# Performance work log

Hardware: AMD Instinct MI355X
Metric: run time of the kernel (lower is better)

The kernel has to match this reference:

```python
import jax, jax.numpy as jnp
import numpy as np

N_EMBD = 1024
N_HEAD = 16
HEAD_DIM = N_EMBD // N_HEAD
D_FF = 4 * N_EMBD
B, T = 2, 2048


def setup_inputs() -> dict:
    key = jax.random.key(0)
    ks = jax.random.split(key, 16)
    s = 0.02
    d = {
        'x': jax.random.normal(ks[0], (B, T, N_EMBD), jnp.float32),
        'ln1_g': jnp.ones((N_EMBD,), jnp.float32),
        'ln1_b': jnp.zeros((N_EMBD,), jnp.float32),
        'Wq': jax.random.normal(ks[1], (N_EMBD, N_EMBD), jnp.float32) * s,
        'bq': jnp.zeros((N_EMBD,), jnp.float32),
        'Wk': jax.random.normal(ks[2], (N_EMBD, N_EMBD), jnp.float32) * s,
        'bk': jnp.zeros((N_EMBD,), jnp.float32),
        'Wv': jax.random.normal(ks[3], (N_EMBD, N_EMBD), jnp.float32) * s,
        'bv': jnp.zeros((N_EMBD,), jnp.float32),
        'Wo': jax.random.normal(ks[4], (N_EMBD, N_EMBD), jnp.float32) * s,
        'bo': jnp.zeros((N_EMBD,), jnp.float32),
        'ln2_g': jnp.ones((N_EMBD,), jnp.float32),
        'ln2_b': jnp.zeros((N_EMBD,), jnp.float32),
        'W1': jax.random.normal(ks[5], (N_EMBD, D_FF), jnp.float32) * s,
        'b1': jnp.zeros((D_FF,), jnp.float32),
        'W2': jax.random.normal(ks[6], (D_FF, N_EMBD), jnp.float32) * s,
        'b2': jnp.zeros((N_EMBD,), jnp.float32),
    }
    return d


def _layernorm(x, g, b, eps=1e-5):
    mu = jnp.mean(x, axis=-1, keepdims=True)
    var = jnp.var(x, axis=-1, keepdims=True)
    return (x - mu) * jax.lax.rsqrt(var + eps) * g + b


def _attention(x, Wq, bq, Wk, bk, Wv, bv, Wo, bo):
    b, t, c = x.shape
    q = (x @ Wq + bq).reshape(b, t, N_HEAD, HEAD_DIM).transpose(0, 2, 1, 3)
    k = (x @ Wk + bk).reshape(b, t, N_HEAD, HEAD_DIM).transpose(0, 2, 1, 3)
    v = (x @ Wv + bv).reshape(b, t, N_HEAD, HEAD_DIM).transpose(0, 2, 1, 3)
    att = jnp.einsum('bhqd,bhkd->bhqk', q, k) / jnp.sqrt(jnp.float32(HEAD_DIM))
    causal = jnp.tril(jnp.ones((t, t), bool))
    att = jnp.where(causal[None, None], att, -jnp.inf)
    att = jax.nn.softmax(att, axis=-1)
    y = jnp.einsum('bhqk,bhkd->bhqd', att, v)
    y = y.transpose(0, 2, 1, 3).reshape(b, t, c)
    return y @ Wo + bo


def reference(x, ln1_g, ln1_b, Wq, bq, Wk, bk, Wv, bv, Wo, bo, ln2_g, ln2_b, W1, b1, W2, b2):
    x = x + _attention(_layernorm(x, ln1_g, ln1_b), Wq, bq, Wk, bk, Wv, bv, Wo, bo)
    h = _layernorm(x, ln2_g, ln2_b)
    h = jax.nn.gelu(h @ W1 + b1, approximate=False) @ W2 + b2
    return x + h
```

## Files before the change

kernel.cpp:

```cpp
#include <hip/hip_runtime.h>
#include <hip/hip_bf16.h>

typedef __hip_bfloat16 bf16;
using bf16x8 = __attribute__((ext_vector_type(8))) short;
using f32x4  = __attribute__((ext_vector_type(4))) float;
using f32x16 = __attribute__((ext_vector_type(16))) float;
using u32x4  = __attribute__((ext_vector_type(4))) unsigned int;

#define TSEQ 2048
#define NH   16
#define HD   64
#define NC   1024
#define DFF  4096
#define NROWS 4096

__device__ __forceinline__ void load_lds16(const bf16* g, bf16* l) {
  __builtin_amdgcn_global_load_lds(
      (const __attribute__((address_space(1))) unsigned int*)g,
      (__attribute__((address_space(3))) unsigned int*)l, 16, 0, 0);
}

__device__ __forceinline__ float b2f(short s) {
  unsigned int u = ((unsigned int)(unsigned short)s) << 16;
  return __builtin_bit_cast(float, u);
}

__device__ __forceinline__ unsigned cvtpk(float a, float b) {
  unsigned r;
  asm("v_cvt_pk_bf16_f32 %0, %1, %2" : "=v"(r) : "v"(a), "v"(b));
  return r;
}

__device__ __forceinline__ void pl32swap(unsigned &d, unsigned &s) {
  asm("v_permlane32_swap_b32 %0, %1" : "+v"(d), "+v"(s));
}

__device__ __forceinline__ float gelu_f(float x) {
  float u = 0.7978845608028654f * fmaf(0.044715f * x, x * x, x);
  float e = __expf(2.0f * u);
  float t = 1.0f - 2.0f / (e + 1.0f);
  return 0.5f * x * (1.0f + t);
}

__global__ __launch_bounds__(256)
void ln_cast_kernel(const float* __restrict__ x, const float* __restrict__ g,
                    const float* __restrict__ b, bf16* __restrict__ out) {
  int row = blockIdx.x, tid = threadIdx.x;
  const float4 v = ((const float4*)(x + (size_t)row * NC))[tid];
  float s  = v.x + v.y + v.z + v.w;
  float s2 = v.x*v.x + v.y*v.y + v.z*v.z + v.w*v.w;
#pragma unroll
  for (int m = 1; m < 64; m <<= 1) { s += __shfl_xor(s, m); s2 += __shfl_xor(s2, m); }
  __shared__ float rs[4], rs2[4];
  if ((tid & 63) == 0) { rs[tid >> 6] = s; rs2[tid >> 6] = s2; }
  __syncthreads();
  s  = rs[0] + rs[1] + rs[2] + rs[3];
  s2 = rs2[0] + rs2[1] + rs2[2] + rs2[3];
  float mu   = s * (1.0f / NC);
  float var  = s2 * (1.0f / NC) - mu * mu;
  float rstd = rsqrtf(var + 1e-5f);
  const float4 gv = ((const float4*)g)[tid];
  const float4 bv = ((const float4*)b)[tid];
  bf16* o = out + (size_t)row * NC + tid * 4;
  o[0] = __float2bfloat16((v.x - mu) * rstd * gv.x + bv.x);
  o[1] = __float2bfloat16((v.y - mu) * rstd * gv.y + bv.y);
  o[2] = __float2bfloat16((v.z - mu) * rstd * gv.z + bv.z);
  o[3] = __float2bfloat16((v.w - mu) * rstd * gv.w + bv.w);
}

__global__ __launch_bounds__(256)
void wo_ln_kernel(const float* __restrict__ x, const float* __restrict__ bo,
                  const bf16* __restrict__ P, const float* __restrict__ g,
                  const float* __restrict__ bln, float* __restrict__ x2,
                  bf16* __restrict__ xn2) {
  int row = blockIdx.x, tid = threadIdx.x;
  size_t base = (size_t)row * NC + tid * 4;
  const float4 xv = *(const float4*)(x + base);
  const float4 bv = ((const float4*)bo)[tid];
  short4 p0 = *(const short4*)((const short*)P + base);
  short4 p1 = *(const short4*)((const short*)P + (size_t)NROWS * NC + base);
  float v0 = xv.x + bv.x + b2f(p0.x) + b2f(p1.x);
  float v1 = xv.y + bv.y + b2f(p0.y) + b2f(p1.y);
  float v2 = xv.z + bv.z + b2f(p0.z) + b2f(p1.z);
  float v3 = xv.w + bv.w + b2f(p0.w) + b2f(p1.w);
  float4 ov = {v0, v1, v2, v3};
  *(float4*)(x2 + base) = ov;
  float s  = v0 + v1 + v2 + v3;
  float s2 = v0*v0 + v1*v1 + v2*v2 + v3*v3;
#pragma unroll
  for (int m = 1; m < 64; m <<= 1) { s += __shfl_xor(s, m); s2 += __shfl_xor(s2, m); }
  __shared__ float rs[4], rs2[4];
  if ((tid & 63) == 0) { rs[tid >> 6] = s; rs2[tid >> 6] = s2; }
  __syncthreads();
  s  = rs[0] + rs[1] + rs[2] + rs[3];
  s2 = rs2[0] + rs2[1] + rs2[2] + rs2[3];
  float mu   = s * (1.0f / NC);
  float var  = s2 * (1.0f / NC) - mu * mu;
  float rstd = rsqrtf(var + 1e-5f);
  const float4 gv = ((const float4*)g)[tid];
  const float4 lv = ((const float4*)bln)[tid];
  bf16* o = xn2 + base;
  o[0] = __float2bfloat16((v0 - mu) * rstd * gv.x + lv.x);
  o[1] = __float2bfloat16((v1 - mu) * rstd * gv.y + lv.y);
  o[2] = __float2bfloat16((v2 - mu) * rstd * gv.z + lv.z);
  o[3] = __float2bfloat16((v3 - mu) * rstd * gv.w + lv.w);
}

__global__ __launch_bounds__(256)
void w2_final_kernel(const float* __restrict__ x2, const float* __restrict__ b2,
                     const bf16* __restrict__ P, float* __restrict__ out) {
  int row = blockIdx.x, tid = threadIdx.x;
  size_t base = (size_t)row * NC + tid * 4;
  const float4 xv = *(const float4*)(x2 + base);
  const float4 bv = ((const float4*)b2)[tid];
  float a0 = xv.x + bv.x, a1 = xv.y + bv.y, a2 = xv.z + bv.z, a3 = xv.w + bv.w;
#pragma unroll
  for (int z = 0; z < 4; ++z) {
    short4 p = *(const short4*)((const short*)P + (size_t)z * NROWS * NC + base);
    a0 += b2f(p.x); a1 += b2f(p.y); a2 += b2f(p.z); a3 += b2f(p.w);
  }
  float4 ov = {a0, a1, a2, a3};
  *(float4*)(out + base) = ov;
}

__global__ __launch_bounds__(256)
void transpose_all_kernel(const float* __restrict__ Wq, const float* __restrict__ Wk,
                          const float* __restrict__ Wv, const float* __restrict__ Wo,
                          const float* __restrict__ W1, const float* __restrict__ W2,
                          bf16* __restrict__ WqkvoT, bf16* __restrict__ W1T,
                          bf16* __restrict__ W2T) {
  int bid = blockIdx.x;
  const float* W; bf16* Wt; int K, N, nx, tile;
  if (bid < 4096) {
    int z = bid >> 10; tile = bid & 1023;
    W = (z == 0) ? Wq : (z == 1) ? Wk : (z == 2) ? Wv : Wo;
    Wt = WqkvoT + (size_t)z * NC * NC; K = NC; N = NC; nx = 32;
  } else if (bid < 8192) {
    tile = bid - 4096; W = W1; Wt = W1T; K = NC; N = DFF; nx = 128;
  } else {
    tile = bid - 8192; W = W2; Wt = W2T; K = DFF; N = NC; nx = 32;
  }
  int n0 = (tile % nx) * 32, k0 = (tile / nx) * 32;
  __shared__ float t[32][33];
  int tx = threadIdx.x, ty = threadIdx.y;
#pragma unroll
  for (int i = 0; i < 4; ++i)
    t[ty + i * 8][tx] = W[(size_t)(k0 + ty + i * 8) * N + n0 + tx];
  __syncthreads();
#pragma unroll
  for (int i = 0; i < 4; ++i)
    Wt[(size_t)(n0 + ty + i * 8) * K + k0 + tx] = __float2bfloat16(t[tx][ty + i * 8]);
}

#define MODE_GELU 4
#define MODE_QKV  5
#define MODE_PART 6

template <int MODE>
__global__ __launch_bounds__(256)
void gemm_bt(const bf16* __restrict__ A, const bf16* __restrict__ Bt,
             const float* __restrict__ bias, const float* __restrict__ bias2,
             const float* __restrict__ bias3,
             void* __restrict__ outp, void* __restrict__ out2, void* __restrict__ out3,
             int M, int N, int K, int KS) {
  __shared__ bf16 As[128 * 64];
  __shared__ bf16 Bs[128 * 64];
  int tid  = threadIdx.x;
  int w    = tid >> 6;
  int lane = tid & 63;
  int l32  = lane & 31;
  int khalf = lane >> 5;
  int sx   = lane & 7;
  int waveM = (w >> 1) * 64, waveN = (w & 1) * 64;

  int gN = gridDim.x, gM = gridDim.y;
  int pid = blockIdx.y * gN + blockIdx.x;
  int npg = 8 * gN;
  int gid = pid / npg;
  int fm  = gid * 8;
  int gsz = min(gM - fm, 8);
  int bm = (fm + (pid % gsz)) * 128;
  int bn = ((pid % npg) / gsz) * 128;

  int k_beg = blockIdx.z * KS;

  const bf16* pA[4]; const bf16* pB[4];
#pragma unroll
  for (int i = 0; i < 4; ++i) {
    int p = i * 256 + tid;
    int row = p >> 3;
    int lc = (p & 7) ^ (row & 7);
    pA[i] = A  + (size_t)(bm + row) * K + k_beg + lc * 8;
    pB[i] = Bt + (size_t)(bn + row) * K + k_beg + lc * 8;
  }

  f32x16 acc[2][2];
#pragma unroll
  for (int mi = 0; mi < 2; ++mi)
#pragma unroll
    for (int ni = 0; ni < 2; ++ni)
#pragma unroll
      for (int r = 0; r < 16; ++r) acc[mi][ni][r] = 0.f;

  for (int kt = 0; kt < KS; kt += 64) {
    __syncthreads();
#pragma unroll
    for (int i = 0; i < 4; ++i) {
      load_lds16(pA[i], &As[(i * 256 + w * 64) * 8]);
      load_lds16(pB[i], &Bs[(i * 256 + w * 64) * 8]);
      pA[i] += 64; pB[i] += 64;
    }
    __syncthreads();
#pragma unroll
    for (int s = 0; s < 4; ++s) {
      int ch = ((s * 2 + khalf) ^ sx) * 8;
      bf16x8 af[2], bfr[2];
#pragma unroll
      for (int mi = 0; mi < 2; ++mi)
        af[mi] = *(const bf16x8*)&As[(waveM + mi * 32 + l32) * 64 + ch];
#pragma unroll
      for (int ni = 0; ni < 2; ++ni)
        bfr[ni] = *(const bf16x8*)&Bs[(waveN + ni * 32 + l32) * 64 + ch];
#pragma unroll
      for (int mi = 0; mi < 2; ++mi)
#pragma unroll
        for (int ni = 0; ni < 2; ++ni)
          acc[mi][ni] = __builtin_amdgcn_mfma_f32_32x32x16_bf16(af[mi], bfr[ni], acc[mi][ni], 0, 0, 0);
    }
  }

  if (MODE == MODE_PART) {
    bf16* dst = (bf16*)outp + (size_t)blockIdx.z * M * N;
#pragma unroll
    for (int mi = 0; mi < 2; ++mi)
#pragma unroll
      for (int ni = 0; ni < 2; ++ni) {
        int col = bn + waveN + ni * 32 + l32;
#pragma unroll
        for (int reg = 0; reg < 16; ++reg) {
          int row = bm + waveM + mi * 32 + (reg & 3) + 8 * (reg >> 2) + 4 * khalf;
          dst[(size_t)row * N + col] = __float2bfloat16(acc[mi][ni][reg]);
        }
      }
  } else if (MODE == MODE_GELU) {
    float bcol[2];
#pragma unroll
    for (int ni = 0; ni < 2; ++ni) bcol[ni] = bias[bn + waveN + ni * 32 + l32];
#pragma unroll
    for (int mi = 0; mi < 2; ++mi)
#pragma unroll
      for (int ni = 0; ni < 2; ++ni) {
        int col = bn + waveN + ni * 32 + l32;
#pragma unroll
        for (int reg = 0; reg < 16; ++reg) {
          int row = bm + waveM + mi * 32 + (reg & 3) + 8 * (reg >> 2) + 4 * khalf;
          ((bf16*)outp)[(size_t)row * N + col] =
              __float2bfloat16(gelu_f(acc[mi][ni][reg] + bcol[ni]));
        }
      }
  } else {
    int seg = bn >> 10;
    int c1b = (bn & (NC - 1)) + waveN;
    const float* bp = (seg == 0) ? bias : (seg == 1) ? bias2 : bias3;
    float bcol[2]; int hh[2], dd[2];
#pragma unroll
    for (int ni = 0; ni < 2; ++ni) {
      int c1 = c1b + ni * 32 + l32;
      bcol[ni] = bp[c1]; hh[ni] = c1 >> 6; dd[ni] = c1 & (HD - 1);
    }
    if (seg == 0) {
      bf16* dst = (bf16*)outp;
#pragma unroll
      for (int mi = 0; mi < 2; ++mi)
#pragma unroll
        for (int reg = 0; reg < 16; ++reg) {
          int row = bm + waveM + mi * 32 + (reg & 3) + 8 * (reg >> 2) + 4 * khalf;
          int bbi = row >> 11, t = row & (TSEQ - 1);
#pragma unroll
          for (int ni = 0; ni < 2; ++ni)
            dst[((size_t)(bbi * NH + hh[ni]) * TSEQ + t) * HD + dd[ni]] =
                __float2bfloat16(acc[mi][ni][reg] + bcol[ni]);
        }
    } else if (seg == 1) {
      bf16* dst = (bf16*)out2;
#pragma unroll
      for (int mi = 0; mi < 2; ++mi)
#pragma unroll
        for (int reg = 0; reg < 16; ++reg) {
          int row = bm + waveM + mi * 32 + (reg & 3) + 8 * (reg >> 2) + 4 * khalf;
          int bbi = row >> 11, t = row & (TSEQ - 1);
          int kt = t >> 5, lk = t & 31;
#pragma unroll
          for (int ni = 0; ni < 2; ++ni) {
            int d = dd[ni];
            size_t off = ((((size_t)(bbi * NH + hh[ni]) * 64 + kt) * 4 + (d >> 4)) * 64
                          + ((d >> 3) & 1) * 32 + lk) * 8 + (d & 7);
            dst[off] = __float2bfloat16(acc[mi][ni][reg] + bcol[ni]);
          }
        }
    } else {
      bf16* dst = (bf16*)out3;
#pragma unroll
      for (int mi = 0; mi < 2; ++mi)
#pragma unroll
        for (int reg = 0; reg < 16; ++reg) {
          int row = bm + waveM + mi * 32 + (reg & 3) + 8 * (reg >> 2) + 4 * khalf;
          int bbi = row >> 11, t = row & (TSEQ - 1);
          int kt = t >> 5, rem = t & 31;
          int ks = rem >> 4, hf = (rem >> 3) & 1, j = rem & 7;
#pragma unroll
          for (int ni = 0; ni < 2; ++ni) {
            int d = dd[ni];
            size_t off = (((((size_t)(bbi * NH + hh[ni]) * 64 + kt) * 2 + (d >> 5)) * 2 + ks) * 64
                          + hf * 32 + (d & 31)) * 8 + j;
            dst[off] = __float2bfloat16(acc[mi][ni][reg] + bcol[ni]);
          }
        }
    }
  }
}

__global__ __launch_bounds__(256)
void attn_kernel(const bf16* __restrict__ q, const bf16* __restrict__ kf,
                 const bf16* __restrict__ vf, bf16* __restrict__ out) {
  int id  = blockIdx.x;
  int xcd = id & 7;
  int t   = id >> 3;
  int bh  = xcd * 4 + (t & 3);
  int u   = t >> 2;
  int qt  = (u < 32) ? (2 * u) : (63 - 2 * (u - 32));
  int b = bh >> 4, h = bh & 15;

  int tid  = threadIdx.x;
  int w    = tid >> 6;
  int lane = tid & 63;
  int l31  = lane & 31;
  int hh   = lane >> 5;
  int h8   = hh * 8;
  int base4 = hh * 4;

  const bf16* qp  = q  + (size_t)(b * NH + h) * TSEQ * HD;
  const bf16* kfb = kf + (size_t)bh * (64 * 4 * 64 * 8);
  const bf16* vfb = vf + (size_t)bh * (64 * 2 * 2 * 64 * 8);

  int q0 = qt * 32;

  bf16x8 qf[4];
#pragma unroll
  for (int ds = 0; ds < 4; ++ds)
    qf[ds] = *(const bf16x8*)(qp + (size_t)(q0 + l31) * HD + ds * 16 + h8);

  f32x16 o0, o1;
#pragma unroll
  for (int r = 0; r < 16; ++r) { o0[r] = 0.f; o1[r] = 0.f; }
  float lacc = 0.f;

  bf16x8 a0, a1, a2, a3;

  auto step = [&](int kt, bool dg) {
    const bf16* vs = vfb + (size_t)kt * 2048 + lane * 8;
    bf16x8 v00 = *(const bf16x8*)(vs);
    bf16x8 v01 = *(const bf16x8*)(vs + 512);
    bf16x8 v10 = *(const bf16x8*)(vs + 1024);
    bf16x8 v11 = *(const bf16x8*)(vs + 1536);
    bf16x8 n0, n1, n2, n3;
    bool pf = !dg && (kt + 4 <= qt);
    if (pf) {
      const bf16* kn = kfb + (size_t)(kt + 4) * 2048 + lane * 8;
      n0 = *(const bf16x8*)(kn);
      n1 = *(const bf16x8*)(kn + 512);
      n2 = *(const bf16x8*)(kn + 1024);
      n3 = *(const bf16x8*)(kn + 1536);
    }

    f32x16 c;
#pragma unroll
    for (int r = 0; r < 16; ++r) c[r] = 0.f;
    c = __builtin_amdgcn_mfma_f32_32x32x16_bf16(a0, qf[0], c, 0, 0, 0);
    c = __builtin_amdgcn_mfma_f32_32x32x16_bf16(a1, qf[1], c, 0, 0, 0);
    c = __builtin_amdgcn_mfma_f32_32x32x16_bf16(a2, qf[2], c, 0, 0, 0);
    c = __builtin_amdgcn_mfma_f32_32x32x16_bf16(a3, qf[3], c, 0, 0, 0);

    float p[16];
    float ls = 0.f;
#pragma unroll
    for (int r = 0; r < 16; ++r) {
      float pv = exp2f(fmaf(c[r], 0.18033688011112042f, -11.541560327111707f));
      if (dg) {
        int krr = (r & 3) + 8 * (r >> 2) + base4;
        pv = (krr <= l31) ? pv : 0.f;
      }
      p[r] = pv;
      ls += pv;
    }
    lacc += ls;

    unsigned A0 = cvtpk(p[0],  p[1]),  C0 = cvtpk(p[4],  p[5]);
    unsigned B0 = cvtpk(p[2],  p[3]),  D0 = cvtpk(p[6],  p[7]);
    pl32swap(A0, C0); pl32swap(B0, D0);
    unsigned A1 = cvtpk(p[8],  p[9]),  C1 = cvtpk(p[12], p[13]);
    unsigned B1 = cvtpk(p[10], p[11]), D1 = cvtpk(p[14], p[15]);
    pl32swap(A1, C1); pl32swap(B1, D1);
    u32x4 w0v = {A0, B0, C0, D0};
    u32x4 w1v = {A1, B1, C1, D1};
    bf16x8 pa0 = __builtin_bit_cast(bf16x8, w0v);
    bf16x8 pa1 = __builtin_bit_cast(bf16x8, w1v);

    o0 = __builtin_amdgcn_mfma_f32_32x32x16_bf16(pa0, v00, o0, 0, 0, 0);
    o0 = __builtin_amdgcn_mfma_f32_32x32x16_bf16(pa1, v01, o0, 0, 0, 0);
    o1 = __builtin_amdgcn_mfma_f32_32x32x16_bf16(pa0, v10, o1, 0, 0, 0);
    o1 = __builtin_amdgcn_mfma_f32_32x32x16_bf16(pa1, v11, o1, 0, 0, 0);

    if (pf) { a0 = n0; a1 = n1; a2 = n2; a3 = n3; }
  };

  if (w <= qt) {
    const bf16* ka = kfb + (size_t)w * 2048 + lane * 8;
    a0 = *(const bf16x8*)(ka);
    a1 = *(const bf16x8*)(ka + 512);
    a2 = *(const bf16x8*)(ka + 1024);
    a3 = *(const bf16x8*)(ka + 1536);
    int diag = (w == (qt & 3)) ? 1 : 0;
    int T = ((qt - w) >> 2) + 1 - diag;
    int kt = w;
    for (int i = 0; i < T; ++i, kt += 4) step(kt, false);
    if (diag) step(qt, true);
  }

  __shared__ float red[2][64][33];
  auto dump = [&](int slot) {
    float* d = &red[slot][lane][0];
#pragma unroll
    for (int r = 0; r < 16; ++r) { d[r] = o0[r]; d[16 + r] = o1[r]; }
    d[32] = lacc;
  };
  auto gather = [&](int slot) {
    const float* s = &red[slot][lane][0];
#pragma unroll
    for (int r = 0; r < 16; ++r) { o0[r] += s[r]; o1[r] += s[16 + r]; }
    lacc += s[32];
  };
  if (w >= 2) dump(w - 2);
  __syncthreads();
  if (w < 2) gather(w);
  __syncthreads();
  if (w == 1) dump(0);
  __syncthreads();
  if (w == 0) {
    gather(0);
    float ltot = lacc + __shfl_xor(lacc, 32);
    float linv = 1.0f / ltot;
#pragma unroll
    for (int r = 0; r < 16; ++r) {
      int qoff = (r & 3) + 8 * (r >> 2) + base4;
      float sc = __shfl(linv, qoff);
      size_t ob = ((size_t)(b * TSEQ + q0 + qoff)) * NC + h * HD + l31;
      out[ob]      = __float2bfloat16(o0[r] * sc);
      out[ob + 32] = __float2bfloat16(o1[r] * sc);
    }
  }
}

extern "C" void kernel_launch(void* const* d_in, const int* in_sizes, int n_in,
                              void* d_out, int out_size, void* d_ws, size_t ws_size,
                              hipStream_t stream) {
  const float* x     = (const float*)d_in[0];
  const float* ln1_g = (const float*)d_in[1];
  const float* ln1_b = (const float*)d_in[2];
  const float* Wq    = (const float*)d_in[3];
  const float* bq    = (const float*)d_in[4];
  const float* Wk    = (const float*)d_in[5];
  const float* bk    = (const float*)d_in[6];
  const float* Wv    = (const float*)d_in[7];
  const float* bv    = (const float*)d_in[8];
  const float* Wo    = (const float*)d_in[9];
  const float* bo    = (const float*)d_in[10];
  const float* ln2_g = (const float*)d_in[11];
  const float* ln2_b = (const float*)d_in[12];
  const float* W1    = (const float*)d_in[13];
  const float* b1    = (const float*)d_in[14];
  const float* W2    = (const float*)d_in[15];
  const float* b2    = (const float*)d_in[16];

  char* ws = (char*)d_ws;
  const size_t MB = 1u << 20;
  bf16* WqkvT = (bf16*)(ws + 0 * MB);
  bf16* W1T  = (bf16*)(ws + 8 * MB);
  bf16* W2T  = (bf16*)(ws + 16 * MB);
  bf16* xn1  = (bf16*)(ws + 24 * MB);
  bf16* qb   = (bf16*)(ws + 32 * MB);
  bf16* kfB  = (bf16*)(ws + 40 * MB);
  bf16* vfB  = (bf16*)(ws + 48 * MB);
  bf16* att  = (bf16*)(ws + 56 * MB);
  float* x2  = (float*)(ws + 64 * MB);
  bf16* xn2  = (bf16*)(ws + 80 * MB);
  bf16* h1   = (bf16*)(ws + 88 * MB);
  bf16* woP  = (bf16*)(ws + 88 * MB);
  bf16* w2P  = (bf16*)(ws + 32 * MB);
  bf16* WoT  = WqkvT + 3 * (size_t)NC * NC;

  transpose_all_kernel<<<12288, dim3(32, 8), 0, stream>>>(
      Wq, Wk, Wv, Wo, W1, W2, WqkvT, W1T, W2T);

  ln_cast_kernel<<<NROWS, 256, 0, stream>>>(x, ln1_g, ln1_b, xn1);

  gemm_bt<MODE_QKV><<<dim3(24, 32, 1), 256, 0, stream>>>(
      xn1, WqkvT, bq, bk, bv, qb, kfB, vfB, NROWS, 3 * NC, NC, NC);

  attn_kernel<<<2048, 256, 0, stream>>>(qb, kfB, vfB, att);

  gemm_bt<MODE_PART><<<dim3(8, 32, 2), 256, 0, stream>>>(
      att, WoT, nullptr, nullptr, nullptr, woP, nullptr, nullptr, NROWS, NC, NC, NC / 2);

  wo_ln_kernel<<<NROWS, 256, 0, stream>>>(x, bo, woP, ln2_g, ln2_b, x2, xn2);

  gemm_bt<MODE_GELU><<<dim3(32, 32, 1), 256, 0, stream>>>(
      xn2, W1T, b1, nullptr, nullptr, h1, nullptr, nullptr, NROWS, DFF, NC, NC);

  gemm_bt<MODE_PART><<<dim3(8, 32, 4), 256, 0, stream>>>(
      h1, W2T, nullptr, nullptr, nullptr, w2P, nullptr, nullptr, NROWS, NC, DFF, DFF / 4);

  w2_final_kernel<<<NROWS, 256, 0, stream>>>(x2, b2, w2P, (float*)d_out);
}
```

Baseline: 340.5 us.

## Replace 128x128 GEMM with 256x256-tile, 512-thread, 4-stage pipelined kernel

Result: slower. 359.4 us (+5.6%).

```diff
diff --git a/kernel.cpp b/kernel.cpp
--- a/kernel.cpp
+++ b/kernel.cpp
@@ -157,124 +157,139 @@
 #define MODE_PART 6
 
 template <int MODE>
-__global__ __launch_bounds__(256)
-void gemm_bt(const bf16* __restrict__ A, const bf16* __restrict__ Bt,
+__global__ __launch_bounds__(512, 2)
+void gemm256(const bf16* __restrict__ A, const bf16* __restrict__ Bt,
              const float* __restrict__ bias, const float* __restrict__ bias2,
              const float* __restrict__ bias3,
              void* __restrict__ outp, void* __restrict__ out2, void* __restrict__ out3,
              int M, int N, int K, int KS) {
-  __shared__ bf16 As[128 * 64];
-  __shared__ bf16 Bs[128 * 64];
+  __shared__ bf16 lds[65536];
   int tid  = threadIdx.x;
   int w    = tid >> 6;
   int lane = tid & 63;
-  int l32  = lane & 31;
-  int khalf = lane >> 5;
-  int sx   = lane & 7;
-  int waveM = (w >> 1) * 64, waveN = (w & 1) * 64;
+  int l31  = lane & 31;
+  int kb   = lane >> 5;
+  int wm   = w >> 2, wn = w & 3;
 
   int gN = gridDim.x, gM = gridDim.y;
   int pid = blockIdx.y * gN + blockIdx.x;
-  int npg = 8 * gN;
+  int npg = 4 * gN;
   int gid = pid / npg;
-  int fm  = gid * 8;
-  int gsz = min(gM - fm, 8);
-  int bm = (fm + (pid % gsz)) * 128;
-  int bn = ((pid % npg) / gsz) * 128;
-
+  int fm  = gid * 4;
+  int gsz = min(gM - fm, 4);
+  int bm = (fm + (pid % gsz)) * 256;
+  int bn = ((pid % npg) / gsz) * 256;
   int k_beg = blockIdx.z * KS;
 
-  const bf16* pA[4]; const bf16* pB[4];
-#pragma unroll
-  for (int i = 0; i < 4; ++i) {
-    int p = i * 256 + tid;
-    int row = p >> 3;
-    int lc = (p & 7) ^ (row & 7);
-    pA[i] = A  + (size_t)(bm + row) * K + k_beg + lc * 8;
-    pB[i] = Bt + (size_t)(bn + row) * K + k_beg + lc * 8;
-  }
-
-  f32x16 acc[2][2];
-#pragma unroll
-  for (int mi = 0; mi < 2; ++mi)
+  int srow  = w * 32 + (lane >> 1);
+  int skoff = (lane & 1) * 8;
+  const bf16* sA[2]; const bf16* sB[2];
+#pragma unroll
+  for (int j = 0; j < 2; ++j) {
+    sA[j] = A  + (size_t)(bm + srow) * K + k_beg + j * 16 + skoff;
+    sB[j] = Bt + (size_t)(bn + srow) * K + k_beg + j * 16 + skoff;
+  }
+
+  auto stage = [&](int t) {
+    int b = t & 3;
+    bf16* dA = &lds[b * 8192];
+    bf16* dB = &lds[32768 + b * 8192];
+    int koff = t * 32;
+#pragma unroll
+    for (int j = 0; j < 2; ++j) {
+      load_lds16(sA[j] + koff, dA + (j * 512 + w * 64) * 8);
+      load_lds16(sB[j] + koff, dB + (j * 512 + w * 64) * 8);
+    }
+  };
+
+  f32x16 acc[4][2];
+#pragma unroll
+  for (int mi = 0; mi < 4; ++mi)
 #pragma unroll
     for (int ni = 0; ni < 2; ++ni)
 #pragma unroll
       for (int r = 0; r < 16; ++r) acc[mi][ni][r] = 0.f;
 
-  for (int kt = 0; kt < KS; kt += 64) {
-    __syncthreads();
-#pragma unroll
-    for (int i = 0; i < 4; ++i) {
-      load_lds16(pA[i], &As[(i * 256 + w * 64) * 8]);
-      load_lds16(pB[i], &Bs[(i * 256 + w * 64) * 8]);
-      pA[i] += 64; pB[i] += 64;
-    }
-    __syncthreads();
-#pragma unroll
-    for (int s = 0; s < 4; ++s) {
-      int ch = ((s * 2 + khalf) ^ sx) * 8;
-      bf16x8 af[2], bfr[2];
-#pragma unroll
-      for (int mi = 0; mi < 2; ++mi)
-        af[mi] = *(const bf16x8*)&As[(waveM + mi * 32 + l32) * 64 + ch];
+  int NT = KS >> 5;
+  stage(0); stage(1); stage(2);
+
+  for (int t = 0; t < NT; ++t) {
+    if (t < NT - 2)       asm volatile("s_waitcnt vmcnt(8)" ::: "memory");
+    else if (t == NT - 2) asm volatile("s_waitcnt vmcnt(4)" ::: "memory");
+    else                  asm volatile("s_waitcnt vmcnt(0)" ::: "memory");
+    __builtin_amdgcn_s_barrier();
+    asm volatile("" ::: "memory");
+    if (t + 3 < NT) stage(t + 3);
+
+    const bf16* bufA = &lds[(t & 3) * 8192];
+    const bf16* bufB = &lds[32768 + (t & 3) * 8192];
+    bf16x8 af[2][4], bfr[2][2];
+#pragma unroll
+    for (int ks = 0; ks < 2; ++ks) {
+#pragma unroll
+      for (int mi = 0; mi < 4; ++mi)
+        af[ks][mi] = *(const bf16x8*)&bufA[(ks * 512 + (wm * 128 + mi * 32 + l31) * 2 + kb) * 8];
 #pragma unroll
       for (int ni = 0; ni < 2; ++ni)
-        bfr[ni] = *(const bf16x8*)&Bs[(waveN + ni * 32 + l32) * 64 + ch];
-#pragma unroll
-      for (int mi = 0; mi < 2; ++mi)
+        bfr[ks][ni] = *(const bf16x8*)&bufB[(ks * 512 + (wn * 64 + ni * 32 + l31) * 2 + kb) * 8];
+    }
+    __builtin_amdgcn_s_setprio(1);
+#pragma unroll
+    for (int ks = 0; ks < 2; ++ks)
+#pragma unroll
+      for (int mi = 0; mi < 4; ++mi)
 #pragma unroll
         for (int ni = 0; ni < 2; ++ni)
-          acc[mi][ni] = __builtin_amdgcn_mfma_f32_32x32x16_bf16(af[mi], bfr[ni], acc[mi][ni], 0, 0, 0);
-    }
+          acc[mi][ni] = __builtin_amdgcn_mfma_f32_32x32x16_bf16(af[ks][mi], bfr[ks][ni], acc[mi][ni], 0, 0, 0);
+    __builtin_amdgcn_s_setprio(0);
   }
 
   if (MODE == MODE_PART) {
     bf16* dst = (bf16*)outp + (size_t)blockIdx.z * M * N;
 #pragma unroll
-    for (int mi = 0; mi < 2; ++mi)
+    for (int mi = 0; mi < 4; ++mi)
 #pragma unroll
       for (int ni = 0; ni < 2; ++ni) {
-        int col = bn + waveN + ni * 32 + l32;
+        int col = bn + wn * 64 + ni * 32 + l31;
 #pragma unroll
         for (int reg = 0; reg < 16; ++reg) {
-          int row = bm + waveM + mi * 32 + (reg & 3) + 8 * (reg >> 2) + 4 * khalf;
+          int row = bm + wm * 128 + mi * 32 + (reg & 3) + 8 * (reg >> 2) + 4 * kb;
           dst[(size_t)row * N + col] = __float2bfloat16(acc[mi][ni][reg]);
         }
       }
   } else if (MODE == MODE_GELU) {
     float bcol[2];
 #pragma unroll
-    for (int ni = 0; ni < 2; ++ni) bcol[ni] = bias[bn + waveN + ni * 32 + l32];
-#pragma unroll
-    for (int mi = 0; mi < 2; ++mi)
+    for (int ni = 0; ni < 2; ++ni) bcol[ni] = bias[bn + wn * 64 + ni * 32 + l31];
+#pragma unroll
+    for (int mi = 0; mi < 4; ++mi)
 #pragma unroll
       for (int ni = 0; ni < 2; ++ni) {
-        int col = bn + waveN + ni * 32 + l32;
+        int col = bn + wn * 64 + ni * 32 + l31;
 #pragma unroll
         for (int reg = 0; reg < 16; ++reg) {
-          int row = bm + waveM + mi * 32 + (reg & 3) + 8 * (reg >> 2) + 4 * khalf;
+          int row = bm + wm * 128 + mi * 32 + (reg & 3) + 8 * (reg >> 2) + 4 * kb;
           ((bf16*)outp)[(size_t)row * N + col] =
               __float2bfloat16(gelu_f(acc[mi][ni][reg] + bcol[ni]));
         }
       }
   } else {
     int seg = bn >> 10;
-    int c1b = (bn & (NC - 1)) + waveN;
+    int c1b = (bn & (NC - 1)) + wn * 64;
     const float* bp = (seg == 0) ? bias : (seg == 1) ? bias2 : bias3;
     float bcol[2]; int hh[2], dd[2];
 #pragma unroll
     for (int ni = 0; ni < 2; ++ni) {
-      int c1 = c1b + ni * 32 + l32;
+      int c1 = c1b + ni * 32 + l31;
       bcol[ni] = bp[c1]; hh[ni] = c1 >> 6; dd[ni] = c1 & (HD - 1);
     }
     if (seg == 0) {
       bf16* dst = (bf16*)outp;
 #pragma unroll
-      for (int mi = 0; mi < 2; ++mi)
+      for (int mi = 0; mi < 4; ++mi)
 #pragma unroll
         for (int reg = 0; reg < 16; ++reg) {
-          int row = bm + waveM + mi * 32 + (reg & 3) + 8 * (reg >> 2) + 4 * khalf;
+          int row = bm + wm * 128 + mi * 32 + (reg & 3) + 8 * (reg >> 2) + 4 * kb;
           int bbi = row >> 11, t = row & (TSEQ - 1);
 #pragma unroll
           for (int ni = 0; ni < 2; ++ni)
@@ -284,10 +299,10 @@
     } else if (seg == 1) {
       bf16* dst = (bf16*)out2;
 #pragma unroll
-      for (int mi = 0; mi < 2; ++mi)
+      for (int mi = 0; mi < 4; ++mi)
 #pragma unroll
         for (int reg = 0; reg < 16; ++reg) {
-          int row = bm + waveM + mi * 32 + (reg & 3) + 8 * (reg >> 2) + 4 * khalf;
+          int row = bm + wm * 128 + mi * 32 + (reg & 3) + 8 * (reg >> 2) + 4 * kb;
           int bbi = row >> 11, t = row & (TSEQ - 1);
           int kt = t >> 5, lk = t & 31;
 #pragma unroll
@@ -301,10 +316,10 @@
     } else {
       bf16* dst = (bf16*)out3;
 #pragma unroll
-      for (int mi = 0; mi < 2; ++mi)
+      for (int mi = 0; mi < 4; ++mi)
 #pragma unroll
         for (int reg = 0; reg < 16; ++reg) {
-          int row = bm + waveM + mi * 32 + (reg & 3) + 8 * (reg >> 2) + 4 * khalf;
+          int row = bm + wm * 128 + mi * 32 + (reg & 3) + 8 * (reg >> 2) + 4 * kb;
           int bbi = row >> 11, t = row & (TSEQ - 1);
           int kt = t >> 5, rem = t & 31;
           int ks = rem >> 4, hf = (rem >> 3) & 1, j = rem & 7;
@@ -504,20 +519,20 @@
 
   ln_cast_kernel<<<NROWS, 256, 0, stream>>>(x, ln1_g, ln1_b, xn1);
 
-  gemm_bt<MODE_QKV><<<dim3(24, 32, 1), 256, 0, stream>>>(
+  gemm256<MODE_QKV><<<dim3(12, 16, 1), 512, 0, stream>>>(
       xn1, WqkvT, bq, bk, bv, qb, kfB, vfB, NROWS, 3 * NC, NC, NC);
 
   attn_kernel<<<2048, 256, 0, stream>>>(qb, kfB, vfB, att);
 
-  gemm_bt<MODE_PART><<<dim3(8, 32, 2), 256, 0, stream>>>(
+  gemm256<MODE_PART><<<dim3(4, 16, 2), 512, 0, stream>>>(
       att, WoT, nullptr, nullptr, nullptr, woP, nullptr, nullptr, NROWS, NC, NC, NC / 2);
 
   wo_ln_kernel<<<NROWS, 256, 0, stream>>>(x, bo, woP, ln2_g, ln2_b, x2, xn2);
 
-  gemm_bt<MODE_GELU><<<dim3(32, 32, 1), 256, 0, stream>>>(
+  gemm256<MODE_GELU><<<dim3(16, 16, 1), 512, 0, stream>>>(
       xn2, W1T, b1, nullptr, nullptr, h1, nullptr, nullptr, NROWS, DFF, NC, NC);
 
-  gemm_bt<MODE_PART><<<dim3(8, 32, 4), 256, 0, stream>>>(
+  gemm256<MODE_PART><<<dim3(4, 16, 4), 512, 0, stream>>>(
       h1, W2T, nullptr, nullptr, nullptr, w2P, nullptr, nullptr, NROWS, NC, DFF, DFF / 4);
 
   w2_final_kernel<<<NROWS, 256, 0, stream>>>(x2, b2, w2P, (float*)d_out);
```
